# Kernel optimization log

Hardware: AMD Instinct MI355X
Metric: run time of the kernel (lower is better)

## Reference

```python
import jax, jax.numpy as jnp
import numpy as np

INIT_STDEV = 0.01

def setup_inputs() -> dict:
    key = jax.random.key(0)
    k1, k2, k3 = jax.random.split(key, 3)
    B, S, D = 8, 4096, 768
    x = jax.random.normal(k1, (B, S, D), dtype=jnp.float32)
    att_v = jax.random.normal(k2, (D,), dtype=jnp.float32) * INIT_STDEV
    att_W = jax.random.normal(k3, (D, D), dtype=jnp.float32) * INIT_STDEV
    return {"x": x, "att_v": att_v, "att_W": att_W}

def reference(x, att_v, att_W):
    # y = x @ W : [B,S,D]; scores = tanh(y) . v over D : [B,S]
    y = jnp.tanh(jnp.einsum('bsd,de->bse', x, att_W))
    scores = jnp.einsum('bsd,d->bs', y, att_v)
    weights = jax.nn.softmax(scores, axis=-1)            # softmax over sequence
    out = jnp.einsum('bs,bsd->bd', weights, x)           # attsum pool
    return out.astype(jnp.float32)
```

## Files before the change

kernel.cpp:

```cpp
#include <hip/hip_runtime.h>
#include <hip/hip_bf16.h>

constexpr int Bb = 8;
constexpr int Ss = 4096;
constexpr int Dd = 768;
constexpr int Mm = Bb * Ss;

constexpr int BM = 64;
constexpr int LDA = Dd + 8;

typedef __bf16 bf16x8 __attribute__((ext_vector_type(8)));
typedef __bf16 bf16x4 __attribute__((ext_vector_type(4)));
typedef float f32x4 __attribute__((ext_vector_type(4)));

__device__ __forceinline__ float fast_tanh(float x) {
    return 1.f - 2.f / (__expf(2.f * x) + 1.f);
}

__global__ __launch_bounds__(256) void convW(const float* __restrict__ W,
                                             __bf16* __restrict__ Wt) {
    __shared__ float tile[32][33];
    const int tx = threadIdx.x & 31;
    const int ty = threadIdx.x >> 5;
    const int kb = blockIdx.x * 32;
    const int nb = blockIdx.y * 32;
#pragma unroll
    for (int i = 0; i < 32; i += 8)
        tile[ty + i][tx] = W[(size_t)(kb + ty + i) * Dd + nb + tx];
    __syncthreads();
#pragma unroll
    for (int i = 0; i < 32; i += 8)
        Wt[(size_t)(nb + ty + i) * Dd + kb + tx] = (__bf16)tile[tx][ty + i];
}

__global__ __launch_bounds__(512, 2) void scores_gemm(
    const float* __restrict__ x, const __bf16* __restrict__ Wt,
    const float* __restrict__ v, float* __restrict__ scores) {
    __shared__ __bf16 As[BM * LDA];
    __shared__ float sc_sh[8][BM];

    const int t = threadIdx.x;
    const int mb = blockIdx.x;
    const int lane = t & 63;
    const int w = t >> 6;
    const int quad = lane >> 4;
    const int lid = lane & 15;

    {
        const float* xb = x + (size_t)mb * BM * Dd;
#pragma unroll
        for (int i = 0; i < 24; ++i) {
            const int f = i * 512 + t;
            const int row = f / 192;
            const int c4 = f - row * 192;
            const float4 a = *(const float4*)(xb + (size_t)row * Dd + c4 * 4);
            bf16x4 p;
            p[0] = (__bf16)a.x; p[1] = (__bf16)a.y; p[2] = (__bf16)a.z; p[3] = (__bf16)a.w;
            *(bf16x4*)(&As[row * LDA + c4 * 4]) = p;
        }
    }
    __syncthreads();

    float racc[4][4];
#pragma unroll
    for (int tm = 0; tm < 4; ++tm)
#pragma unroll
        for (int r = 0; r < 4; ++r) racc[tm][r] = 0.f;

#pragma unroll
    for (int iter = 0; iter < 2; ++iter) {
        const int colbase = iter * 384 + w * 48;
        const __bf16* wp0 = Wt + (size_t)(colbase + 0  + lid) * Dd + quad * 8;
        const __bf16* wp1 = Wt + (size_t)(colbase + 16 + lid) * Dd + quad * 8;
        const __bf16* wp2 = Wt + (size_t)(colbase + 32 + lid) * Dd + quad * 8;

        f32x4 acc[4][3];
#pragma unroll
        for (int tm = 0; tm < 4; ++tm)
#pragma unroll
            for (int nt = 0; nt < 3; ++nt) acc[tm][nt] = (f32x4){0.f, 0.f, 0.f, 0.f};

        bf16x8 b0 = *(const bf16x8*)(wp0);
        bf16x8 b1 = *(const bf16x8*)(wp1);
        bf16x8 b2 = *(const bf16x8*)(wp2);

#pragma unroll
        for (int kb = 0; kb < 24; ++kb) {
            bf16x8 n0, n1, n2;
            if (kb < 23) {
                n0 = *(const bf16x8*)(wp0 + (kb + 1) * 32);
                n1 = *(const bf16x8*)(wp1 + (kb + 1) * 32);
                n2 = *(const bf16x8*)(wp2 + (kb + 1) * 32);
            }
            bf16x8 af[4];
#pragma unroll
            for (int tm = 0; tm < 4; ++tm)
                af[tm] = *(const bf16x8*)(&As[(tm * 16 + lid) * LDA + kb * 32 + quad * 8]);
#pragma unroll
            for (int tm = 0; tm < 4; ++tm) {
                acc[tm][0] = __builtin_amdgcn_mfma_f32_16x16x32_bf16(af[tm], b0, acc[tm][0], 0, 0, 0);
                acc[tm][1] = __builtin_amdgcn_mfma_f32_16x16x32_bf16(af[tm], b1, acc[tm][1], 0, 0, 0);
                acc[tm][2] = __builtin_amdgcn_mfma_f32_16x16x32_bf16(af[tm], b2, acc[tm][2], 0, 0, 0);
            }
            b0 = n0; b1 = n1; b2 = n2;
        }

        const float v0 = v[colbase + 0 + lid];
        const float v1 = v[colbase + 16 + lid];
        const float v2 = v[colbase + 32 + lid];
#pragma unroll
        for (int tm = 0; tm < 4; ++tm)
#pragma unroll
            for (int r = 0; r < 4; ++r)
                racc[tm][r] += v0 * fast_tanh(acc[tm][0][r])
                             + v1 * fast_tanh(acc[tm][1][r])
                             + v2 * fast_tanh(acc[tm][2][r]);
    }

#pragma unroll
    for (int tm = 0; tm < 4; ++tm)
#pragma unroll
        for (int r = 0; r < 4; ++r) {
            float s = racc[tm][r];
            s += __shfl_xor(s, 1);
            s += __shfl_xor(s, 2);
            s += __shfl_xor(s, 4);
            s += __shfl_xor(s, 8);
            if (lid == 0) sc_sh[w][tm * 16 + quad * 4 + r] = s;
        }
    __syncthreads();
    if (t < BM) {
        float s = 0.f;
#pragma unroll
        for (int ww = 0; ww < 8; ++ww) s += sc_sh[ww][t];
        scores[mb * BM + t] = s;
    }
}

__global__ __launch_bounds__(256) void pool_k(const float* __restrict__ x,
                                              const float* __restrict__ scores,
                                              float* __restrict__ out) {
    const int b = blockIdx.y;
    const int sc = blockIdx.x;
    const int t = threadIdx.x;
    const float* srow = scores + (size_t)b * Ss;
    __shared__ float red[256];

    float mx = -1e30f;
    for (int i = t; i < Ss; i += 256) mx = fmaxf(mx, srow[i]);
    red[t] = mx;
    __syncthreads();
    for (int o = 128; o > 0; o >>= 1) {
        if (t < o) red[t] = fmaxf(red[t], red[t + o]);
        __syncthreads();
    }
    mx = red[0];
    __syncthreads();
    float sum = 0.f;
    for (int i = t; i < Ss; i += 256) sum += __expf(srow[i] - mx);
    red[t] = sum;
    __syncthreads();
    for (int o = 128; o > 0; o >>= 1) {
        if (t < o) red[t] += red[t + o];
        __syncthreads();
    }
    const float inv = 1.f / red[0];

    float a0 = 0.f, a1 = 0.f, a2 = 0.f;
    const int s0 = sc * 128;
#pragma unroll 4
    for (int i = 0; i < 128; ++i) {
        const int s = s0 + i;
        const float ww = __expf(srow[s] - mx) * inv;
        const float* xr = x + ((size_t)b * Ss + s) * Dd;
        a0 += ww * xr[t];
        a1 += ww * xr[t + 256];
        a2 += ww * xr[t + 512];
    }
    float* o = out + (size_t)b * Dd;
    atomicAdd(o + t, a0);
    atomicAdd(o + t + 256, a1);
    atomicAdd(o + t + 512, a2);
}

extern "C" void kernel_launch(void* const* d_in, const int* in_sizes, int n_in,
                              void* d_out, int out_size, void* d_ws, size_t ws_size,
                              hipStream_t stream) {
    (void)in_sizes; (void)n_in; (void)ws_size;
    const float* x = (const float*)d_in[0];
    const float* v = (const float*)d_in[1];
    const float* W = (const float*)d_in[2];

    char* ws = (char*)d_ws;
    __bf16* Wt = (__bf16*)ws;
    float* scores = (float*)(ws + 1179648);

    hipMemsetAsync(d_out, 0, (size_t)out_size * sizeof(float), stream);

    convW<<<dim3(Dd / 32, Dd / 32), 256, 0, stream>>>(W, Wt);
    scores_gemm<<<dim3(Mm / BM), 512, 0, stream>>>(x, Wt, v, scores);
    pool_k<<<dim3(32, Bb), 256, 0, stream>>>(x, scores, d_out ? (float*)d_out : nullptr);
}
```

Before: 250.8 us.

## Pipeline x-chunk loads with MFMA in scores GEMM and split softmax from pooling

The scores GEMM now loads x in four K-chunks through registers and stores each chunk to a fragment-ordered LDS layout while the previous chunk's MFMAs run. Each wave covers 96 output columns in a single pass instead of two passes of 48, which removes the second pass over the A tile. Softmax moves into its own kernel that writes normalized weights, so the pooling kernel stops recomputing the max and sum reductions in every block. Pooling now uses float4 loads over 1024 blocks. The cost is more accumulator registers, an extra launch and more atomics.

```diff
diff --git a/kernel.cpp b/kernel.cpp
--- a/kernel.cpp
+++ b/kernel.cpp
@@ -7,7 +7,7 @@
 constexpr int Mm = Bb * Ss;
 
 constexpr int BM = 64;
-constexpr int LDA = Dd + 8;
+constexpr int KCH = 4;
 
 typedef __bf16 bf16x8 __attribute__((ext_vector_type(8)));
 typedef __bf16 bf16x4 __attribute__((ext_vector_type(4)));
@@ -36,7 +36,7 @@
 __global__ __launch_bounds__(512, 2) void scores_gemm(
     const float* __restrict__ x, const __bf16* __restrict__ Wt,
     const float* __restrict__ v, float* __restrict__ scores) {
-    __shared__ __bf16 As[BM * LDA];
+    __shared__ __bf16 As[24 * 4 * 64 * 8];
     __shared__ float sc_sh[8][BM];
 
     const int t = threadIdx.x;
@@ -46,82 +46,103 @@
     const int quad = lane >> 4;
     const int lid = lane & 15;
 
-    {
-        const float* xb = x + (size_t)mb * BM * Dd;
-#pragma unroll
-        for (int i = 0; i < 24; ++i) {
-            const int f = i * 512 + t;
-            const int row = f / 192;
-            const int c4 = f - row * 192;
-            const float4 a = *(const float4*)(xb + (size_t)row * Dd + c4 * 4);
+    const float* xb = x + (size_t)mb * BM * Dd;
+
+    float4 sreg[6];
+    auto load_chunk = [&](int c) {
+#pragma unroll
+        for (int j = 0; j < 6; ++j) {
+            const int idx = j * 512 + t;
+            const int row = idx / 48;
+            const int c4 = idx - row * 48;
+            sreg[j] = *(const float4*)(xb + (size_t)row * Dd + c * 192 + c4 * 4);
+        }
+    };
+    auto store_chunk = [&](int c) {
+#pragma unroll
+        for (int j = 0; j < 6; ++j) {
+            const int idx = j * 512 + t;
+            const int row = idx / 48;
+            const int c4 = idx - row * 48;
+            const int k0 = c * 192 + c4 * 4;
+            const int kb = k0 >> 5;
+            const int qd = (k0 >> 3) & 3;
+            const int j0 = k0 & 7;
+            const int tm = row >> 4;
+            const int ld = row & 15;
             bf16x4 p;
-            p[0] = (__bf16)a.x; p[1] = (__bf16)a.y; p[2] = (__bf16)a.z; p[3] = (__bf16)a.w;
-            *(bf16x4*)(&As[row * LDA + c4 * 4]) = p;
-        }
-    }
-    __syncthreads();
-
-    float racc[4][4];
+            p[0] = (__bf16)sreg[j].x; p[1] = (__bf16)sreg[j].y;
+            p[2] = (__bf16)sreg[j].z; p[3] = (__bf16)sreg[j].w;
+            *(bf16x4*)(&As[(((kb * 4 + tm) * 64) + qd * 16 + ld) * 8 + j0]) = p;
+        }
+    };
+
+    const __bf16* wp[6];
+#pragma unroll
+    for (int nt = 0; nt < 6; ++nt)
+        wp[nt] = Wt + (size_t)(w * 96 + nt * 16 + lid) * Dd + quad * 8;
+
+    f32x4 acc[4][6];
 #pragma unroll
     for (int tm = 0; tm < 4; ++tm)
 #pragma unroll
-        for (int r = 0; r < 4; ++r) racc[tm][r] = 0.f;
-
-#pragma unroll
-    for (int iter = 0; iter < 2; ++iter) {
-        const int colbase = iter * 384 + w * 48;
-        const __bf16* wp0 = Wt + (size_t)(colbase + 0  + lid) * Dd + quad * 8;
-        const __bf16* wp1 = Wt + (size_t)(colbase + 16 + lid) * Dd + quad * 8;
-        const __bf16* wp2 = Wt + (size_t)(colbase + 32 + lid) * Dd + quad * 8;
-
-        f32x4 acc[4][3];
-#pragma unroll
-        for (int tm = 0; tm < 4; ++tm)
-#pragma unroll
-            for (int nt = 0; nt < 3; ++nt) acc[tm][nt] = (f32x4){0.f, 0.f, 0.f, 0.f};
-
-        bf16x8 b0 = *(const bf16x8*)(wp0);
-        bf16x8 b1 = *(const bf16x8*)(wp1);
-        bf16x8 b2 = *(const bf16x8*)(wp2);
-
-#pragma unroll
-        for (int kb = 0; kb < 24; ++kb) {
-            bf16x8 n0, n1, n2;
-            if (kb < 23) {
-                n0 = *(const bf16x8*)(wp0 + (kb + 1) * 32);
-                n1 = *(const bf16x8*)(wp1 + (kb + 1) * 32);
-                n2 = *(const bf16x8*)(wp2 + (kb + 1) * 32);
+        for (int nt = 0; nt < 6; ++nt) acc[tm][nt] = (f32x4){0.f, 0.f, 0.f, 0.f};
+
+    load_chunk(0);
+    store_chunk(0);
+
+    bf16x8 bcur[6], bnxt[6];
+#pragma unroll
+    for (int nt = 0; nt < 6; ++nt) bcur[nt] = *(const bf16x8*)(wp[nt]);
+
+    bf16x8 afc[4], afn[4];
+
+    for (int c = 0; c < KCH; ++c) {
+        __syncthreads();
+        if (c < KCH - 1) load_chunk(c + 1);
+        {
+            const int kb = c * 6;
+#pragma unroll
+            for (int tm = 0; tm < 4; ++tm)
+                afc[tm] = *(const bf16x8*)(&As[((kb * 4 + tm) * 64 + lane) * 8]);
+        }
+#pragma unroll
+        for (int kk = 0; kk < 6; ++kk) {
+            const int kb = c * 6 + kk;
+            if (kb + 1 < 24) {
+#pragma unroll
+                for (int nt = 0; nt < 6; ++nt)
+                    bnxt[nt] = *(const bf16x8*)(wp[nt] + (kb + 1) * 32);
             }
-            bf16x8 af[4];
+            if (kk < 5) {
+#pragma unroll
+                for (int tm = 0; tm < 4; ++tm)
+                    afn[tm] = *(const bf16x8*)(&As[(((kb + 1) * 4 + tm) * 64 + lane) * 8]);
+            }
 #pragma unroll
             for (int tm = 0; tm < 4; ++tm)
-                af[tm] = *(const bf16x8*)(&As[(tm * 16 + lid) * LDA + kb * 32 + quad * 8]);
-#pragma unroll
-            for (int tm = 0; tm < 4; ++tm) {
-                acc[tm][0] = __builtin_amdgcn_mfma_f32_16x16x32_bf16(af[tm], b0, acc[tm][0], 0, 0, 0);
-                acc[tm][1] = __builtin_amdgcn_mfma_f32_16x16x32_bf16(af[tm], b1, acc[tm][1], 0, 0, 0);
-                acc[tm][2] = __builtin_amdgcn_mfma_f32_16x16x32_bf16(af[tm], b2, acc[tm][2], 0, 0, 0);
-            }
-            b0 = n0; b1 = n1; b2 = n2;
-        }
-
-        const float v0 = v[colbase + 0 + lid];
-        const float v1 = v[colbase + 16 + lid];
-        const float v2 = v[colbase + 32 + lid];
-#pragma unroll
-        for (int tm = 0; tm < 4; ++tm)
-#pragma unroll
-            for (int r = 0; r < 4; ++r)
-                racc[tm][r] += v0 * fast_tanh(acc[tm][0][r])
-                             + v1 * fast_tanh(acc[tm][1][r])
-                             + v2 * fast_tanh(acc[tm][2][r]);
-    }
+#pragma unroll
+                for (int nt = 0; nt < 6; ++nt)
+                    acc[tm][nt] = __builtin_amdgcn_mfma_f32_16x16x32_bf16(afc[tm], bcur[nt], acc[tm][nt], 0, 0, 0);
+#pragma unroll
+            for (int tm = 0; tm < 4; ++tm) afc[tm] = afn[tm];
+#pragma unroll
+            for (int nt = 0; nt < 6; ++nt) bcur[nt] = bnxt[nt];
+        }
+        if (c < KCH - 1) store_chunk(c + 1);
+    }
+
+    float vv[6];
+#pragma unroll
+    for (int nt = 0; nt < 6; ++nt) vv[nt] = v[w * 96 + nt * 16 + lid];
 
 #pragma unroll
     for (int tm = 0; tm < 4; ++tm)
 #pragma unroll
         for (int r = 0; r < 4; ++r) {
-            float s = racc[tm][r];
+            float s = 0.f;
+#pragma unroll
+            for (int nt = 0; nt < 6; ++nt) s += vv[nt] * fast_tanh(acc[tm][nt][r]);
             s += __shfl_xor(s, 1);
             s += __shfl_xor(s, 2);
             s += __shfl_xor(s, 4);
@@ -137,50 +158,63 @@
     }
 }
 
-__global__ __launch_bounds__(256) void pool_k(const float* __restrict__ x,
-                                              const float* __restrict__ scores,
+__global__ __launch_bounds__(256) void softmax_k(const float* __restrict__ scores,
+                                                 float* __restrict__ weights) {
+    const int b = blockIdx.x;
+    const int t = threadIdx.x;
+    const float* s = scores + (size_t)b * Ss;
+    float* wgt = weights + (size_t)b * Ss;
+    __shared__ float red[256];
+
+    float mx = -1e30f;
+    for (int i = t; i < Ss; i += 256) mx = fmaxf(mx, s[i]);
+    red[t] = mx;
+    __syncthreads();
+    for (int o = 128; o > 0; o >>= 1) {
+        if (t < o) red[t] = fmaxf(red[t], red[t + o]);
+        __syncthreads();
+    }
+    mx = red[0];
+    __syncthreads();
+    float sum = 0.f;
+    for (int i = t; i < Ss; i += 256) {
+        const float e = __expf(s[i] - mx);
+        wgt[i] = e;
+        sum += e;
+    }
+    red[t] = sum;
+    __syncthreads();
+    for (int o = 128; o > 0; o >>= 1) {
+        if (t < o) red[t] += red[t + o];
+        __syncthreads();
+    }
+    const float inv = 1.f / red[0];
+    for (int i = t; i < Ss; i += 256) wgt[i] *= inv;
+}
+
+__global__ __launch_bounds__(192) void pool_k(const float* __restrict__ x,
+                                              const float* __restrict__ weights,
                                               float* __restrict__ out) {
     const int b = blockIdx.y;
     const int sc = blockIdx.x;
     const int t = threadIdx.x;
-    const float* srow = scores + (size_t)b * Ss;
-    __shared__ float red[256];
-
-    float mx = -1e30f;
-    for (int i = t; i < Ss; i += 256) mx = fmaxf(mx, srow[i]);
-    red[t] = mx;
-    __syncthreads();
-    for (int o = 128; o > 0; o >>= 1) {
-        if (t < o) red[t] = fmaxf(red[t], red[t + o]);
-        __syncthreads();
-    }
-    mx = red[0];
-    __syncthreads();
-    float sum = 0.f;
-    for (int i = t; i < Ss; i += 256) sum += __expf(srow[i] - mx);
-    red[t] = sum;
-    __syncthreads();
-    for (int o = 128; o > 0; o >>= 1) {
-        if (t < o) red[t] += red[t + o];
-        __syncthreads();
-    }
-    const float inv = 1.f / red[0];
-
-    float a0 = 0.f, a1 = 0.f, a2 = 0.f;
-    const int s0 = sc * 128;
-#pragma unroll 4
-    for (int i = 0; i < 128; ++i) {
+    const int s0 = sc * 32;
+    float4 acc = make_float4(0.f, 0.f, 0.f, 0.f);
+#pragma unroll 8
+    for (int i = 0; i < 32; ++i) {
         const int s = s0 + i;
-        const float ww = __expf(srow[s] - mx) * inv;
-        const float* xr = x + ((size_t)b * Ss + s) * Dd;
-        a0 += ww * xr[t];
-        a1 += ww * xr[t + 256];
-        a2 += ww * xr[t + 512];
-    }
-    float* o = out + (size_t)b * Dd;
-    atomicAdd(o + t, a0);
-    atomicAdd(o + t + 256, a1);
-    atomicAdd(o + t + 512, a2);
+        const float ww = weights[(size_t)b * Ss + s];
+        const float4 xv = *(const float4*)(x + ((size_t)b * Ss + s) * Dd + t * 4);
+        acc.x += ww * xv.x;
+        acc.y += ww * xv.y;
+        acc.z += ww * xv.z;
+        acc.w += ww * xv.w;
+    }
+    float* o = out + (size_t)b * Dd + t * 4;
+    atomicAdd(o + 0, acc.x);
+    atomicAdd(o + 1, acc.y);
+    atomicAdd(o + 2, acc.z);
+    atomicAdd(o + 3, acc.w);
 }
 
 extern "C" void kernel_launch(void* const* d_in, const int* in_sizes, int n_in,
@@ -194,10 +228,12 @@
     char* ws = (char*)d_ws;
     __bf16* Wt = (__bf16*)ws;
     float* scores = (float*)(ws + 1179648);
+    float* weights = (float*)(ws + 1179648 + 131072);
 
     hipMemsetAsync(d_out, 0, (size_t)out_size * sizeof(float), stream);
 
     convW<<<dim3(Dd / 32, Dd / 32), 256, 0, stream>>>(W, Wt);
     scores_gemm<<<dim3(Mm / BM), 512, 0, stream>>>(x, Wt, v, scores);
-    pool_k<<<dim3(32, Bb), 256, 0, stream>>>(x, scores, d_out ? (float*)d_out : nullptr);
-}
+    softmax_k<<<dim3(Bb), 256, 0, stream>>>(scores, weights);
+    pool_k<<<dim3(128, Bb), 192, 0, stream>>>(x, weights, (float*)d_out);
+}
```

After: 271.8 us. 8.4% more time.
